# Kernel tuning notes

Measured on AMD Instinct MI355X. Metric: run time of the kernel, lower is better.

Reference implementation:

```python
import jax, jax.numpy as jnp
import numpy as np

B, T, C, H, W = 1, 8, 64, 96, 96
DG = 16  # deform groups
MAX_RES = 5.0  # max_residue_magnitude


def lrelu(x):
    return jnp.where(x >= 0, x, 0.1 * x)


def conv(x, w, b):
    y = jax.lax.conv_general_dilated(x, w, (1, 1), 'SAME',
                                     dimension_numbers=('NCHW', 'OIHW', 'NCHW'))
    return y + b[None, :, None, None]


def mod_deform_conv2d(x, offset, mask, weight, bias, dg):
    # Modulated deformable conv v2: 3x3 kernel, stride 1, pad 1, dil 1.
    Bs, Cin, Hs, Ws = x.shape
    K = 9
    cpg = Cin // dg
    Cout = weight.shape[0]
    off = offset.reshape(Bs, dg, K, 2, Hs, Ws)  # (y, x) per tap
    m = mask.reshape(Bs, dg, K, Hs, Ws)
    ky = jnp.repeat(jnp.arange(3), 3).astype(x.dtype)
    kx = jnp.tile(jnp.arange(3), 3).astype(x.dtype)
    # base sampling positions: out_pos - pad + tap*dil
    py = (jnp.arange(Hs, dtype=x.dtype) - 1.0)[None, :, None] + ky[:, None, None]  # (K,H,1)
    px = (jnp.arange(Ws, dtype=x.dtype) - 1.0)[None, None, :] + kx[:, None, None]  # (K,1,W)
    sy = off[:, :, :, 0] + py  # (B,dg,K,H,W)
    sx = off[:, :, :, 1] + px
    y0 = jnp.floor(sy)
    x0 = jnp.floor(sx)
    fy = sy - y0
    fx = sx - x0
    y0i = y0.astype(jnp.int32)
    x0i = x0.astype(jnp.int32)
    xf = x.reshape(Bs, dg, cpg, Hs * Ws)

    def gather(yi, xi, wgt):
        valid = (yi >= 0) & (yi < Hs) & (xi >= 0) & (xi < Ws)
        idx = (jnp.clip(yi, 0, Hs - 1) * Ws + jnp.clip(xi, 0, Ws - 1))
        idx = idx.reshape(Bs, dg, 1, K * Hs * Ws)
        v = jnp.take_along_axis(xf, idx, axis=3).reshape(Bs, dg, cpg, K, Hs, Ws)
        return v * (wgt * valid)[:, :, None]

    val = (gather(y0i, x0i, (1 - fy) * (1 - fx))
           + gather(y0i, x0i + 1, (1 - fy) * fx)
           + gather(y0i + 1, x0i, fy * (1 - fx))
           + gather(y0i + 1, x0i + 1, fy * fx))
    cols = val * m[:, :, None]  # (B,dg,cpg,K,H,W)
    wr = weight.reshape(Cout, dg, cpg, K)
    out = jnp.einsum('ogck,bgckhw->bohw', wr, cols)
    return out + bias[None, :, None, None]


def deform_align(xin, cond, p):
    h = lrelu(conv(cond, p['ow1'], p['ob1']))
    h = lrelu(conv(h, p['ow2'], p['ob2']))
    h = lrelu(conv(h, p['ow3'], p['ob3']))
    out = conv(h, p['ow4'], p['ob4'])
    offset = MAX_RES * jnp.tanh(out[:, :18 * DG])
    mask = jax.nn.sigmoid(out[:, 18 * DG:])
    return mod_deform_conv2d(xin, offset, mask, p['dw'], p['db'], DG)


def bidir_prop(x, params):
    t = x.shape[1]
    spatial = [x[:, i] for i in range(t)]
    feats = {}
    for name, rev in (('backward_', True), ('forward_', False)):
        p = params[name]
        order = list(range(t))[::-1] if rev else list(range(t))
        out_list = []
        prop = jnp.zeros_like(spatial[0])
        for i, idx in enumerate(order):
            cur = spatial[idx]
            if i > 0:
                feat_n2 = out_list[-2] if i > 1 else jnp.zeros_like(prop)
                cond = jnp.concatenate([prop, cur, feat_n2], axis=1)
                prop = deform_align(jnp.concatenate([prop, feat_n2], axis=1), cond, p)
            if name == 'forward_':
                feat = jnp.concatenate([cur, feats['backward_'][idx], prop], axis=1)
            else:
                feat = jnp.concatenate([cur, prop], axis=1)
            prop = prop + conv(lrelu(conv(feat, p['bw1'], p['bb1'])), p['bw2'], p['bb2'])
            out_list.append(prop)
        feats[name] = out_list[::-1] if rev else out_list
    fw, fb = params['fusion']
    outs = [conv(jnp.concatenate([feats['backward_'][i], feats['forward_'][i]], axis=1), fw, fb)
            for i in range(t)]
    return jnp.stack(outs, axis=1) + x


def setup_inputs() -> dict:
    key = jax.random.key(0)
    ks = iter(jax.random.split(key, 64))

    def w(*shape):
        return jax.random.normal(next(ks), shape, jnp.float32) * 0.03

    def b(n):
        return jnp.zeros((n,), jnp.float32)

    d = {'x': jax.random.normal(next(ks), (B, T, C, H, W), jnp.float32)}
    for pre, bb1_in in (('b', 2 * C), ('f', 3 * C)):
        d[pre + '_dw'] = w(C, 2 * C, 3, 3); d[pre + '_db'] = b(C)
        d[pre + '_ow1'] = w(C, 3 * C, 3, 3); d[pre + '_ob1'] = b(C)
        d[pre + '_ow2'] = w(C, C, 3, 3); d[pre + '_ob2'] = b(C)
        d[pre + '_ow3'] = w(C, C, 3, 3); d[pre + '_ob3'] = b(C)
        d[pre + '_ow4'] = w(27 * DG, C, 3, 3); d[pre + '_ob4'] = b(27 * DG)
        d[pre + '_bw1'] = w(C, bb1_in, 3, 3); d[pre + '_bb1'] = b(C)
        d[pre + '_bw2'] = w(C, C, 3, 3); d[pre + '_bb2'] = b(C)
    d['fus_w'] = w(C, 2 * C, 1, 1)
    d['fus_b'] = b(C)
    return d


def _assemble(b_dw, b_db, b_ow1, b_ob1, b_ow2, b_ob2, b_ow3, b_ob3, b_ow4, b_ob4,
              b_bw1, b_bb1, b_bw2, b_bb2,
              f_dw, f_db, f_ow1, f_ob1, f_ow2, f_ob2, f_ow3, f_ob3, f_ow4, f_ob4,
              f_bw1, f_bb1, f_bw2, f_bb2, fus_w, fus_b):
    return {
        'backward_': dict(dw=b_dw, db=b_db, ow1=b_ow1, ob1=b_ob1, ow2=b_ow2, ob2=b_ob2,
                          ow3=b_ow3, ob3=b_ob3, ow4=b_ow4, ob4=b_ob4,
                          bw1=b_bw1, bb1=b_bb1, bw2=b_bw2, bb2=b_bb2),
        'forward_': dict(dw=f_dw, db=f_db, ow1=f_ow1, ob1=f_ob1, ow2=f_ow2, ob2=f_ob2,
                         ow3=f_ow3, ob3=f_ob3, ow4=f_ow4, ob4=f_ob4,
                         bw1=f_bw1, bb1=f_bb1, bw2=f_bw2, bb2=f_bb2),
        'fusion': (fus_w, fus_b),
    }


def reference(x, b_dw, b_db, b_ow1, b_ob1, b_ow2, b_ob2, b_ow3, b_ob3, b_ow4, b_ob4,
              b_bw1, b_bb1, b_bw2, b_bb2,
              f_dw, f_db, f_ow1, f_ob1, f_ow2, f_ob2, f_ow3, f_ob3, f_ow4, f_ob4,
              f_bw1, f_bb1, f_bw2, f_bb2, fus_w, fus_b):
    params = _assemble(b_dw, b_db, b_ow1, b_ob1, b_ow2, b_ob2, b_ow3, b_ob3, b_ow4, b_ob4,
                       b_bw1, b_bb1, b_bw2, b_bb2,
                       f_dw, f_db, f_ow1, f_ob1, f_ow2, f_ob2, f_ow3, f_ob3, f_ow4, f_ob4,
                       f_bw1, f_bb1, f_bw2, f_bb2, fus_w, fus_b)
    return bidir_prop(x, params)
```

## Files before the change

kernel.cpp:

```cpp
#include <hip/hip_runtime.h>
#include <cstddef>
#include <cstdint>

#define HW96 9216
#define FRAME (64 * 9216)

typedef unsigned short ushort_t;
typedef __attribute__((ext_vector_type(8))) short bf16x8;
typedef __attribute__((ext_vector_type(4))) float f32x4;
typedef __attribute__((ext_vector_type(4))) unsigned u32x4;
typedef __attribute__((ext_vector_type(8))) ushort_t u16x8;
typedef __attribute__((ext_vector_type(4))) ushort_t u16x4;

__device__ __forceinline__ void split16(float v, ushort_t& h, ushort_t& l) {
    unsigned u = __float_as_uint(v);
    h = (ushort_t)(u >> 16);
    float rem = v - __uint_as_float(u & 0xFFFF0000u);
    unsigned r = __float_as_uint(rem);
    l = (ushort_t)((r + 0x7FFFu + ((r >> 16) & 1u)) >> 16);
}
__device__ __forceinline__ ushort_t bf16rnd(float v) {
    unsigned u = __float_as_uint(v);
    return (ushort_t)((u + 0x7FFFu + ((u >> 16) & 1u)) >> 16);
}
__device__ __forceinline__ float bfh(ushort_t h) {
    return __uint_as_float(((unsigned)h) << 16);
}

struct FragJob { const float* src; ushort_t* dst; int O, I, OT, KC, mode; };
struct FragJobs { FragJob j[15]; };

__global__ __launch_bounds__(256) void frag_all_k(FragJobs jobs) {
    const FragJob& J = jobs.j[blockIdx.y];
    int idx = blockIdx.x * 256 + threadIdx.x;
    int total = ((J.mode == 0) ? 9 : 1) * J.KC * J.OT * 512;
    if (idx >= total) return;
    int jj = idx & 7;
    int lane = (idx >> 3) & 63;
    int rem = idx >> 9;
    int ot = rem % J.OT;
    rem /= J.OT;
    int cc = rem % J.KC;
    int t = rem / J.KC;
    int o = ot * 16 + (lane & 15);
    float wv = 0.f;
    if (J.mode == 0) {
        int ci = cc * 32 + (lane >> 4) * 8 + jj;
        if (o < J.O && ci < J.I) wv = J.src[(o * J.I + ci) * 9 + t];
    } else if (J.mode == 1) {
        int K = cc * 32 + (lane >> 4) * 8 + jj;
        int g = K / 72, r2 = K % 72;
        int tap = r2 >> 3, c = r2 & 7;
        int ci = g * 8 + c;
        if (o < J.O && ci < J.I) wv = J.src[(o * J.I + ci) * 9 + tap];
    } else {
        int ci = cc * 32 + (lane >> 4) * 8 + jj;
        if (o < J.O && ci < J.I) wv = J.src[o * J.I + ci];
    }
    ushort_t h, l;
    split16(wv, h, l);
    J.dst[idx] = h;
    J.dst[total + idx] = l;
}

__global__ __launch_bounds__(256) void pack_tr_k(const float* __restrict__ src,
                                                 ushort_t* __restrict__ dsth) {
    const int t = blockIdx.y;
    const int px0 = blockIdx.x * 64;
    __shared__ ushort_t tile[64 * 65];
    const float* s = src + (size_t)t * FRAME;
    ushort_t* dh = dsth + (size_t)t * FRAME;
#pragma unroll
    for (int it = 0; it < 16; ++it) {
        int e = it * 256 + threadIdx.x;
        int p = e & 63, ch = e >> 6;
        tile[ch * 65 + p] = bf16rnd(s[(size_t)ch * HW96 + px0 + p]);
    }
    __syncthreads();
#pragma unroll
    for (int it = 0; it < 16; ++it) {
        int e = it * 256 + threadIdx.x;
        int ch = e & 63, p = e >> 6;
        dh[(size_t)(px0 + p) * 64 + ch] = tile[ch * 65 + p];
    }
}

__global__ __launch_bounds__(128, 3) void convh_k(
    const ushort_t* __restrict__ s0, const ushort_t* __restrict__ s1,
    const ushort_t* __restrict__ s2, int b0, int b1, int b2, int nsrc,
    const ushort_t* __restrict__ wfrag, int KCfull,
    const float* __restrict__ bias, ushort_t* __restrict__ outhi, int act) {
    const int tid = threadIdx.x;
    const int lane = tid & 63;
    const int w = tid >> 6;
    const int h = blockIdx.x & 1;
    const int bseg = blockIdx.x >> 1;
    const int ot = h * 2 + w;
    const int xb = (bseg % 6) * 16;
    const int y = bseg / 6;
    const int n = lane & 15;
    const int quad = lane >> 4;

    __shared__ __align__(16) ushort_t ldsH[3 * 18 * 72];

    int jst[4], jok[4], joff[4], jbase[4];
#pragma unroll
    for (int i = 0; i < 4; ++i) {
        int e = tid + i * 128;
        int rc = e >> 3, cg = e & 7;
        int r = rc / 18, col = rc - r * 18;
        int gy = y - 1 + r, gx = xb - 1 + col;
        jst[i] = (e < 432);
        jok[i] = jst[i] && ((unsigned)gy < 96u) && ((unsigned)gx < 96u);
        joff[i] = (gy * 96 + gx) * 64 + cg * 8;
        jbase[i] = rc * 72 + cg * 8;
    }

    f32x4 acc0, acc1;
#pragma unroll
    for (int r = 0; r < 4; ++r) { acc0[r] = 0.f; acc1[r] = 0.f; }

    for (int j = 0; j < nsrc; ++j) {
        const ushort_t* sv = (j == 0) ? s0 : (j == 1 ? s1 : s2);
        const int base = (j == 0) ? b0 : (j == 1 ? b1 : b2);
        __syncthreads();
#pragma unroll
        for (int i = 0; i < 4; ++i) {
            if (jst[i]) {
                u16x8 a;
                if (jok[i]) {
                    a = *(const u16x8*)(sv + joff[i]);
                } else {
#pragma unroll
                    for (int q = 0; q < 8; ++q) a[q] = 0;
                }
                *(u16x8*)(ldsH + jbase[i]) = a;
            }
        }
        __syncthreads();
        bf16x8 pAh[5], pBh[5];
#pragma unroll
        for (int s = 0; s < 23; ++s) {
            if (s >= 5) {
                const int u = s - 5;
                const bf16x8 Ah = pAh[u % 5];
                const bf16x8 Bh = pBh[u % 5];
                if (u & 1)
                    acc1 = __builtin_amdgcn_mfma_f32_16x16x32_bf16(Ah, Bh, acc1, 0, 0, 0);
                else
                    acc0 = __builtin_amdgcn_mfma_f32_16x16x32_bf16(Ah, Bh, acc0, 0, 0, 0);
            }
            if (s < 18) {
                const int t = s >> 1, cc2 = s & 1;
                const int ky = t / 3, kx = t % 3;
                const int ccor = base + cc2;
                const ushort_t* ab =
                    wfrag + (((size_t)(t * KCfull + ccor) * 4 + ot) * 64 + lane) * 8;
                pAh[s % 5] = *(const bf16x8*)ab;
                const int lb = (ky * 18 + n + kx) * 72 + cc2 * 32 + quad * 8;
                pBh[s % 5] = *(const bf16x8*)(ldsH + lb);
            }
        }
    }

    const int px = y * 96 + xb + n;
    u16x4 hi4;
#pragma unroll
    for (int r = 0; r < 4; ++r) {
        int cout = ot * 16 + quad * 4 + r;
        float v = acc0[r] + acc1[r] + bias[cout];
        if (act) v = (v >= 0.f) ? v : 0.1f * v;
        hi4[r] = bf16rnd(v);
    }
    *(u16x4*)(outhi + (size_t)px * 64 + ot * 16 + quad * 4) = hi4;
}

__global__ __launch_bounds__(128, 3) void convb_k(
    const ushort_t* __restrict__ s0, const ushort_t* __restrict__ s1,
    int nsrc, int dslot, const float* __restrict__ dpacc,
    const float* __restrict__ ddbias, const ushort_t* __restrict__ wfrag,
    int KCfull, const float* __restrict__ bias,
    const float* __restrict__ addsrc, const float* __restrict__ addsrc2,
    const float* __restrict__ abias, ushort_t* __restrict__ outhi, int act) {
    const int tid = threadIdx.x;
    const int lane = tid & 63;
    const int w = tid >> 6;
    const int h = blockIdx.x & 1;
    const int bseg = blockIdx.x >> 1;
    const int ot = h * 2 + w;
    const int xb = (bseg % 6) * 16;
    const int y = bseg / 6;
    const int n = lane & 15;
    const int quad = lane >> 4;

    __shared__ __align__(16) ushort_t ldsH[3 * 18 * 72];

    int jst[4], jok[4], joff[4], jbase[4];
#pragma unroll
    for (int i = 0; i < 4; ++i) {
        int e = tid + i * 128;
        int rc = e >> 3, cg = e & 7;
        int r = rc / 18, col = rc - r * 18;
        int gy = y - 1 + r, gx = xb - 1 + col;
        jst[i] = (e < 432);
        jok[i] = jst[i] && ((unsigned)gy < 96u) && ((unsigned)gx < 96u);
        joff[i] = (gy * 96 + gx) * 64 + cg * 8;
        jbase[i] = rc * 72 + cg * 8;
    }

    f32x4 acc0, acc1;
#pragma unroll
    for (int r = 0; r < 4; ++r) { acc0[r] = 0.f; acc1[r] = 0.f; }

    for (int j = 0; j < nsrc; ++j) {
        const int base = j * 2;
        __syncthreads();
        if (j == dslot) {
#pragma unroll
            for (int i = 0; i < 4; ++i) {
                if (jst[i]) {
                    u16x8 a;
                    if (jok[i]) {
                        const int cg8 = ((tid + i * 128) & 7) << 3;
                        f32x4 a0 = *(const f32x4*)(dpacc + joff[i]);
                        f32x4 a1 = *(const f32x4*)(dpacc + joff[i] + 4);
                        f32x4 b0 = *(const f32x4*)(dpacc + FRAME + joff[i]);
                        f32x4 b1 = *(const f32x4*)(dpacc + FRAME + joff[i] + 4);
                        f32x4 d0 = *(const f32x4*)(ddbias + cg8);
                        f32x4 d1 = *(const f32x4*)(ddbias + cg8 + 4);
#pragma unroll
                        for (int q = 0; q < 4; ++q) {
                            a[q] = bf16rnd(a0[q] + b0[q] + d0[q]);
                            a[4 + q] = bf16rnd(a1[q] + b1[q] + d1[q]);
                        }
                    } else {
#pragma unroll
                        for (int q = 0; q < 8; ++q) a[q] = 0;
                    }
                    *(u16x8*)(ldsH + jbase[i]) = a;
                }
            }
        } else {
            const ushort_t* sv = (j == 0) ? s0 : s1;
#pragma unroll
            for (int i = 0; i < 4; ++i) {
                if (jst[i]) {
                    u16x8 a;
                    if (jok[i]) {
                        a = *(const u16x8*)(sv + joff[i]);
                    } else {
#pragma unroll
                        for (int q = 0; q < 8; ++q) a[q] = 0;
                    }
                    *(u16x8*)(ldsH + jbase[i]) = a;
                }
            }
        }
        __syncthreads();
        bf16x8 pAh[5], pBh[5];
#pragma unroll
        for (int s = 0; s < 23; ++s) {
            if (s >= 5) {
                const int u = s - 5;
                const bf16x8 Ah = pAh[u % 5];
                const bf16x8 Bh = pBh[u % 5];
                if (u & 1)
                    acc1 = __builtin_amdgcn_mfma_f32_16x16x32_bf16(Ah, Bh, acc1, 0, 0, 0);
                else
                    acc0 = __builtin_amdgcn_mfma_f32_16x16x32_bf16(Ah, Bh, acc0, 0, 0, 0);
            }
            if (s < 18) {
                const int t = s >> 1, cc2 = s & 1;
                const int ky = t / 3, kx = t % 3;
                const int ccor = j * 2 + cc2;
                (void)ccor;
                const int cco = base + cc2;
                const ushort_t* ab =
                    wfrag + (((size_t)(t * KCfull + cco) * 4 + ot) * 64 + lane) * 8;
                pAh[s % 5] = *(const bf16x8*)ab;
                const int lb = (ky * 18 + n + kx) * 72 + cc2 * 32 + quad * 8;
                pBh[s % 5] = *(const bf16x8*)(ldsH + lb);
            }
        }
    }

    const int px = y * 96 + xb + n;
    f32x4 pa, pb;
#pragma unroll
    for (int r = 0; r < 4; ++r) { pa[r] = 0.f; pb[r] = 0.f; }
    if (addsrc) {
        pa = *(const f32x4*)(addsrc + (size_t)px * 64 + ot * 16 + quad * 4);
        pb = *(const f32x4*)(addsrc2 + (size_t)px * 64 + ot * 16 + quad * 4);
    }
    u16x4 hi4;
#pragma unroll
    for (int r = 0; r < 4; ++r) {
        int cout = ot * 16 + quad * 4 + r;
        float v = acc0[r] + acc1[r] + bias[cout];
        if (act) v = (v >= 0.f) ? v : 0.1f * v;
        if (addsrc) v += pa[r] + pb[r] + abias[cout];
        hi4[r] = bf16rnd(v);
    }
    *(u16x4*)(outhi + (size_t)px * 64 + ot * 16 + quad * 4) = hi4;
}

__global__ __launch_bounds__(256) void dconv_fused_k(
    const ushort_t* __restrict__ sAh, const ushort_t* __restrict__ sBh,
    const ushort_t* __restrict__ hAh, const ushort_t* __restrict__ w4,
    const float* __restrict__ ob4, const ushort_t* __restrict__ dwf,
    int ngr4, float* __restrict__ pacc) {
    const int tid = threadIdx.x;
    const int lane = tid & 63;
    const int w = tid >> 6;
    const int h = blockIdx.x & 1;
    const int seg = blockIdx.x >> 1;
    const int xb = (seg % 6) * 16;
    const int y = seg / 6;
    const int n = lane & 15;
    const int quad = lane >> 4;

    __shared__ __align__(16) char smem[15232 + 9472];
    float* rawS = (float*)smem;
    ushort_t* ldsAH = (ushort_t*)(smem + 15232);
    ushort_t* colsH = (ushort_t*)(smem + 15232);

    const int nrounds = ngr4 >> 1;
    const int ng = nrounds * 4;
    const int g0 = h * ng;
    const int otO_s = (g0 * 18) >> 4;
    const int otO_e = (g0 * 18 + ng * 18 - 1) >> 4;
    const int nO = otO_e - otO_s + 1;
    const int otM_s = (288 + g0 * 9) >> 4;
    const int otM_e = (288 + g0 * 9 + ng * 9 - 1) >> 4;
    const int nM = otM_e - otM_s + 1;
    const int nt = nO + nM;
    const int rowOffO = otO_s * 16;
    const int rowOffM = otM_s * 16 - nO * 16;

#pragma unroll
    for (int i = 0; i < 2; ++i) {
        int e = tid + i * 256;
        if (e < 432) {
            int rc = e >> 3, cg = e & 7;
            int r = rc / 18, col = rc - r * 18;
            int gy = y - 1 + r, gx = xb - 1 + col;
            bool ok = ((unsigned)gy < 96u) && ((unsigned)gx < 96u);
            u16x8 a;
            if (ok) {
                a = *(const u16x8*)(hAh + (gy * 96 + gx) * 64 + cg * 8);
            } else {
#pragma unroll
                for (int q = 0; q < 8; ++q) a[q] = 0;
            }
            *(u16x8*)(ldsAH + rc * 72 + cg * 8) = a;
        }
    }
    __syncthreads();

#pragma unroll 1
    for (int j = 0; j < 4; ++j) {
        const int idx = j * 4 + w;
        if (idx >= nt) break;
        const int ot = (idx < nO) ? (otO_s + idx) : (otM_s + (idx - nO));
        f32x4 a0, a1;
#pragma unroll
        for (int r = 0; r < 4; ++r) { a0[r] = 0.f; a1[r] = 0.f; }
        bf16x8 pAh[5], pBh[5];
#pragma unroll
        for (int s = 0; s < 23; ++s) {
            if (s >= 5) {
                const int u = s - 5;
                const bf16x8 Ah = pAh[u % 5];
                const bf16x8 Bh = pBh[u % 5];
                if (u & 1)
                    a1 = __builtin_amdgcn_mfma_f32_16x16x32_bf16(Ah, Bh, a1, 0, 0, 0);
                else
                    a0 = __builtin_amdgcn_mfma_f32_16x16x32_bf16(Ah, Bh, a0, 0, 0, 0);
            }
            if (s < 18) {
                const int t = s >> 1, cc2 = s & 1;
                const int ky = t / 3, kx = t % 3;
                const ushort_t* ab =
                    w4 + (((size_t)s * 28 + ot) * 64 + lane) * 8;
                pAh[s % 5] = *(const bf16x8*)ab;
                const int lb = (ky * 18 + n + kx) * 72 + cc2 * 32 + quad * 8;
                pBh[s % 5] = *(const bf16x8*)(ldsAH + lb);
            }
        }
#pragma unroll
        for (int r = 0; r < 4; ++r) {
            int cout = ot * 16 + quad * 4 + r;
            float v = a0[r] + a1[r] + (cout < 432 ? ob4[cout] : 0.f);
            rawS[(idx * 16 + quad * 4 + r) * 17 + n] = v;
        }
    }

    f32x4 acc0, acc1;
#pragma unroll
    for (int r = 0; r < 4; ++r) { acc0[r] = 0.f; acc1[r] = 0.f; }

    for (int gci = 0; gci < nrounds; ++gci) {
        const int gc = h * nrounds + gci;
        __syncthreads();
#pragma unroll
        for (int i = 0; i < 3; ++i) {
            int e = tid + i * 256;
            if (e < 576) {
                int p = e & 15;
                int r = e >> 4;
                int gl = r / 9, k = r - gl * 9;
                int g = gc * 4 + gl;
                float ry = rawS[(g * 18 + k * 2 + 0 - rowOffO) * 17 + p];
                float rx = rawS[(g * 18 + k * 2 + 1 - rowOffO) * 17 + p];
                float rm = rawS[(288 + g * 9 + k - rowOffM) * 17 + p];
                float oy = 5.f * (1.f - 2.f / (1.f + __expf(2.f * ry)));
                float ox = 5.f * (1.f - 2.f / (1.f + __expf(2.f * rx)));
                float m = 1.f / (1.f + __expf(-rm));
                float sy = oy + (float)(y - 1 + k / 3);
                float sx = ox + (float)(xb + p - 1 + k % 3);
                float fy0 = floorf(sy), fx0 = floorf(sx);
                float fy = sy - fy0, fx = sx - fx0;
                int y0 = (int)fy0, x0 = (int)fx0;
                int y1 = y0 + 1, x1 = x0 + 1;
                bool vy0 = (unsigned)y0 < 96u, vy1 = (unsigned)y1 < 96u;
                bool vx0 = (unsigned)x0 < 96u, vx1 = (unsigned)x1 < 96u;
                int cy0 = min(max(y0, 0), 95), cy1 = min(max(y1, 0), 95);
                int cx0 = min(max(x0, 0), 95), cx1 = min(max(x1, 0), 95);
                float w00 = (1.f - fy) * (1.f - fx) * ((vy0 && vx0) ? 1.f : 0.f);
                float w01 = (1.f - fy) * fx * ((vy0 && vx1) ? 1.f : 0.f);
                float w10 = fy * (1.f - fx) * ((vy1 && vx0) ? 1.f : 0.f);
                float w11 = fy * fx * ((vy1 && vx1) ? 1.f : 0.f);
                const ushort_t* src = (g < 8) ? sAh : sBh;
                int cb = (g & 7) * 8;
                int kbase = p * 296 + gl * 72 + k * 8;
                ushort_t hh[8];
                if (src) {
                    u16x8 c00 = *(const u16x8*)(src + (cy0 * 96 + cx0) * 64 + cb);
                    u16x8 c01 = *(const u16x8*)(src + (cy0 * 96 + cx1) * 64 + cb);
                    u16x8 c10 = *(const u16x8*)(src + (cy1 * 96 + cx0) * 64 + cb);
                    u16x8 c11 = *(const u16x8*)(src + (cy1 * 96 + cx1) * 64 + cb);
#pragma unroll
                    for (int c = 0; c < 8; ++c) {
                        float v = w00 * bfh(c00[c]) + w01 * bfh(c01[c]) +
                                  w10 * bfh(c10[c]) + w11 * bfh(c11[c]);
                        hh[c] = bf16rnd(v * m);
                    }
                } else {
#pragma unroll
                    for (int c = 0; c < 8; ++c) hh[c] = 0;
                }
                u32x4 H;
#pragma unroll
                for (int q = 0; q < 4; ++q)
                    H[q] = (unsigned)hh[2 * q] | ((unsigned)hh[2 * q + 1] << 16);
                *(u32x4*)(colsH + kbase) = H;
            }
        }
        __syncthreads();
        bf16x8 qAh[4], qBh[4];
#pragma unroll
        for (int s = 0; s < 13; ++s) {
            if (s >= 4) {
                const int u = s - 4;
                const bf16x8 Ah = qAh[u % 4];
                const bf16x8 Bh = qBh[u % 4];
                if (u & 1)
                    acc1 = __builtin_amdgcn_mfma_f32_16x16x32_bf16(Ah, Bh, acc1, 0, 0, 0);
                else
                    acc0 = __builtin_amdgcn_mfma_f32_16x16x32_bf16(Ah, Bh, acc0, 0, 0, 0);
            }
            if (s < 9) {
                const int cc = gc * 9 + s;
                const ushort_t* ab = dwf + (((size_t)cc * 4 + w) * 64 + lane) * 8;
                qAh[s % 4] = *(const bf16x8*)ab;
                const int lb = n * 296 + s * 32 + quad * 8;
                qBh[s % 4] = *(const bf16x8*)(colsH + lb);
            }
        }
    }

    const int pidx = y * 96 + xb + n;
    f32x4 sv;
#pragma unroll
    for (int r = 0; r < 4; ++r) sv[r] = acc0[r] + acc1[r];
    *(f32x4*)(pacc + (size_t)h * FRAME + (size_t)pidx * 64 + w * 16 +
              quad * 4) = sv;
}

__global__ __launch_bounds__(128) void fusem_k(
    const ushort_t* __restrict__ featBh, const ushort_t* __restrict__ featFh,
    const float* __restrict__ x, const ushort_t* __restrict__ wfrag,
    const float* __restrict__ bias, float* __restrict__ out) {
    const int tid = threadIdx.x;
    const int lane = tid & 63;
    const int w = tid >> 6;
    const int h = blockIdx.x & 1;
    const int bseg = blockIdx.x >> 1;
    const int t = blockIdx.y;
    const int ot = h * 2 + w;
    const int xb = (bseg % 6) * 16;
    const int y = bseg / 6;
    const int n = lane & 15;
    const int quad = lane >> 4;

    __shared__ __align__(16) ushort_t ldsH[16 * 144];

    const int p = tid >> 3, cg = tid & 7;
    const int off = ((y * 96 + xb + p) * 64 + cg * 8);
#pragma unroll
    for (int i = 0; i < 2; ++i) {
        const ushort_t* sv =
            (i == 0 ? featBh : featFh) + (size_t)t * FRAME;
        u16x8 a = *(const u16x8*)(sv + off);
        *(u16x8*)(ldsH + p * 144 + i * 64 + cg * 8) = a;
    }
    __syncthreads();

    f32x4 acc0, acc1;
#pragma unroll
    for (int r = 0; r < 4; ++r) { acc0[r] = 0.f; acc1[r] = 0.f; }
    const size_t hlOff = (size_t)4 * 4 * 512;
#pragma unroll
    for (int cc = 0; cc < 4; ++cc) {
        const ushort_t* ab = wfrag + (((size_t)cc * 4 + ot) * 64 + lane) * 8;
        bf16x8 Ah = *(const bf16x8*)ab;
        bf16x8 Al = *(const bf16x8*)(ab + hlOff);
        int lb = n * 144 + cc * 32 + quad * 8;
        bf16x8 Bh = *(const bf16x8*)(ldsH + lb);
        if (cc & 1) {
            acc1 = __builtin_amdgcn_mfma_f32_16x16x32_bf16(Ah, Bh, acc1, 0, 0, 0);
            acc1 = __builtin_amdgcn_mfma_f32_16x16x32_bf16(Al, Bh, acc1, 0, 0, 0);
        } else {
            acc0 = __builtin_amdgcn_mfma_f32_16x16x32_bf16(Ah, Bh, acc0, 0, 0, 0);
            acc0 = __builtin_amdgcn_mfma_f32_16x16x32_bf16(Al, Bh, acc0, 0, 0, 0);
        }
    }

    const int pidx = y * 96 + xb + n;
    const float* xt = x + (size_t)t * FRAME;
    float* od = out + (size_t)t * FRAME;
#pragma unroll
    for (int r = 0; r < 4; ++r) {
        int cout = ot * 16 + quad * 4 + r;
        size_t o2 = (size_t)cout * HW96 + pidx;
        od[o2] = acc0[r] + acc1[r] + bias[cout] + xt[o2];
    }
}

extern "C" void kernel_launch(void* const* d_in, const int* in_sizes, int n_in,
                              void* d_out, int out_size, void* d_ws,
                              size_t ws_size, hipStream_t stream) {
    const float* x = (const float*)d_in[0];
    auto gp = [&](int i) { return (const float*)d_in[i]; };

    struct DirP {
        const float *dw, *db, *ow1, *ob1, *ow2, *ob2, *ow3, *ob3, *ow4, *ob4,
            *bw1, *bb1, *bw2, *bb2;
    };
    DirP Pb{gp(1), gp(2), gp(3), gp(4), gp(5), gp(6), gp(7),
            gp(8), gp(9), gp(10), gp(11), gp(12), gp(13), gp(14)};
    DirP Pf{gp(15), gp(16), gp(17), gp(18), gp(19), gp(20), gp(21),
            gp(22), gp(23), gp(24), gp(25), gp(26), gp(27), gp(28)};
    const float* fus_w = gp(29);
    const float* fus_b = gp(30);

    ushort_t* xh = (ushort_t*)d_ws;
    ushort_t* featBh = xh + (size_t)8 * FRAME;
    ushort_t* featFh = featBh + (size_t)8 * FRAME;
    ushort_t* hAh = featFh + (size_t)8 * FRAME;
    ushort_t* hBh = hAh + FRAME;
    float* pacc = (float*)((((uintptr_t)(hBh + FRAME)) + 15) & ~(uintptr_t)15);
    ushort_t* fragp = (ushort_t*)(pacc + (size_t)2 * FRAME);

    auto falloc = [&](size_t nelem) {
        ushort_t* p = fragp;
        fragp += nelem;
        return p;
    };

    struct DirW { ushort_t *ow1, *ow2, *ow3, *ow4, *bw1, *bw2, *dw; int bw1KC; };
    FragJobs fj;
    int nf = 0;
    auto fjob = [&](const float* src, int O, int I, int OT, int KC) {
        ushort_t* dst = falloc((size_t)2 * 9 * KC * OT * 512);
        fj.j[nf++] = FragJob{src, dst, O, I, OT, KC, 0};
        return dst;
    };
    auto fjobd = [&](const float* src) {
        ushort_t* dst = falloc((size_t)2 * 36 * 4 * 512);
        fj.j[nf++] = FragJob{src, dst, 64, 128, 4, 36, 1};
        return dst;
    };
    DirW Wb, Wf;
    Wb.ow1 = fjob(Pb.ow1, 64, 192, 4, 6);
    Wb.ow2 = fjob(Pb.ow2, 64, 64, 4, 2);
    Wb.ow3 = fjob(Pb.ow3, 64, 64, 4, 2);
    Wb.ow4 = fjob(Pb.ow4, 432, 64, 28, 2);
    Wb.bw1 = fjob(Pb.bw1, 64, 128, 4, 4);
    Wb.bw1KC = 4;
    Wb.bw2 = fjob(Pb.bw2, 64, 64, 4, 2);
    Wb.dw = fjobd(Pb.dw);
    Wf.ow1 = fjob(Pf.ow1, 64, 192, 4, 6);
    Wf.ow2 = fjob(Pf.ow2, 64, 64, 4, 2);
    Wf.ow3 = fjob(Pf.ow3, 64, 64, 4, 2);
    Wf.ow4 = fjob(Pf.ow4, 432, 64, 28, 2);
    Wf.bw1 = fjob(Pf.bw1, 64, 192, 4, 6);
    Wf.bw1KC = 6;
    Wf.bw2 = fjob(Pf.bw2, 64, 64, 4, 2);
    Wf.dw = fjobd(Pf.dw);
    ushort_t* Wfus = falloc((size_t)2 * 4 * 4 * 512);
    fj.j[nf++] = FragJob{fus_w, Wfus, 64, 128, 4, 4, 2};
    frag_all_k<<<dim3(1008, 15), 256, 0, stream>>>(fj);

    pack_tr_k<<<dim3(144, 8), 256, 0, stream>>>(x, xh);

    auto convh = [&](const ushort_t* a, const ushort_t* b, const ushort_t* c2,
                     const ushort_t* frag, int KCfull, const float* bias,
                     ushort_t* out, int act) {
        const ushort_t* srcs[3] = {a, b, c2};
        const ushort_t* S[3] = {nullptr, nullptr, nullptr};
        int B[3] = {0, 0, 0};
        int ns = 0;
        for (int j = 0; j < 3; ++j)
            if (srcs[j]) {
                S[ns] = srcs[j];
                B[ns] = j * 2;
                ++ns;
            }
        convh_k<<<1152, 128, 0, stream>>>(S[0], S[1], S[2], B[0], B[1], B[2],
                                          ns, frag, KCfull, bias, out, act);
    };

    auto convb = [&](const ushort_t* a, const ushort_t* b, int withD,
                     const float* ddbias, const ushort_t* frag, int KCfull,
                     const float* bias, const float* add, const float* add2,
                     const float* abias, ushort_t* out, int act) {
        const ushort_t* S[2] = {nullptr, nullptr};
        int ns = 0;
        if (a) S[ns++] = a;
        if (b) S[ns++] = b;
        int dslot = -1;
        if (withD) { dslot = ns; ++ns; }
        convb_k<<<1152, 128, 0, stream>>>(S[0], S[1], ns, dslot, pacc, ddbias,
                                          frag, KCfull, bias, add, add2,
                                          abias, out, act);
    };

    for (int dir = 0; dir < 2; ++dir) {
        const DirP& P = dir ? Pf : Pb;
        const DirW& W = dir ? Wf : Wb;
        ushort_t* feath = dir ? featFh : featBh;
        const ushort_t* prev1h = nullptr;
        const ushort_t* prev2h = nullptr;
        for (int i = 0; i < 8; ++i) {
            int idx = dir ? i : 7 - i;
            const ushort_t* curh = xh + (size_t)idx * FRAME;
            bool hasD = false;
            if (i > 0) {
                convh(prev1h, curh, prev2h, W.ow1, 6, P.ob1, hAh, 1);
                convh(hAh, nullptr, nullptr, W.ow2, 2, P.ob2, hBh, 1);
                convh(hBh, nullptr, nullptr, W.ow3, 2, P.ob3, hAh, 1);
                int ngr4 = (prev2h != nullptr) ? 4 : 2;
                dconv_fused_k<<<1152, 256, 0, stream>>>(
                    prev1h, prev2h, hAh, W.ow4, P.ob4, W.dw, ngr4, pacc);
                hasD = true;
            }
            ushort_t* dsth = feath + (size_t)idx * FRAME;
            if (dir == 0) {
                convb(curh, nullptr, hasD ? 1 : 0, P.db, W.bw1, W.bw1KC,
                      P.bb1, nullptr, nullptr, nullptr, hBh, 1);
            } else {
                convb(curh, featBh + (size_t)idx * FRAME, hasD ? 1 : 0, P.db,
                      W.bw1, W.bw1KC, P.bb1, nullptr, nullptr, nullptr, hBh,
                      1);
            }
            convb(hBh, nullptr, 0, nullptr, W.bw2, 2, P.bb2,
                  hasD ? pacc : nullptr, pacc + FRAME, P.db, dsth, 0);
            prev2h = prev1h;
            prev1h = dsth;
        }
    }

    fusem_k<<<dim3(1152, 8), 128, 0, stream>>>(featBh, featFh, x, Wfus,
                                               fus_b, (float*)d_out);
}
```

Baseline: 1.063 ms.

## Split deform conv across one block per group-chunk with per-chunk partial buffers

The fused deformable conv kernel now launches one block per 4-group chunk (576*ngr4 blocks) instead of two blocks that each loop over several chunks. Each block computes only the offset/mask tiles it needs and writes its own partial sum buffer. The downstream conv kernels then sum a variable number of partials, and the pacc buffer grows to four frames. This adds parallelism and cuts LDS per block, at the cost of redundant loading and offset-conv work per block and more partial reads downstream.

```diff
diff --git a/kernel.cpp b/kernel.cpp
--- a/kernel.cpp
+++ b/kernel.cpp
@@ -177,10 +177,9 @@
 
 __global__ __launch_bounds__(128, 3) void convb_k(
     const ushort_t* __restrict__ s0, const ushort_t* __restrict__ s1,
-    int nsrc, int dslot, const float* __restrict__ dpacc,
+    int nsrc, int dslot, const float* __restrict__ dpacc, int npacc,
     const float* __restrict__ ddbias, const ushort_t* __restrict__ wfrag,
-    int KCfull, const float* __restrict__ bias,
-    const float* __restrict__ addsrc, const float* __restrict__ addsrc2,
+    int KCfull, const float* __restrict__ bias, int addn,
     const float* __restrict__ abias, ushort_t* __restrict__ outhi, int act) {
     const int tid = threadIdx.x;
     const int lane = tid & 63;
@@ -222,16 +221,17 @@
                     u16x8 a;
                     if (jok[i]) {
                         const int cg8 = ((tid + i * 128) & 7) << 3;
-                        f32x4 a0 = *(const f32x4*)(dpacc + joff[i]);
-                        f32x4 a1 = *(const f32x4*)(dpacc + joff[i] + 4);
-                        f32x4 b0 = *(const f32x4*)(dpacc + FRAME + joff[i]);
-                        f32x4 b1 = *(const f32x4*)(dpacc + FRAME + joff[i] + 4);
-                        f32x4 d0 = *(const f32x4*)(ddbias + cg8);
-                        f32x4 d1 = *(const f32x4*)(ddbias + cg8 + 4);
+                        f32x4 v0 = *(const f32x4*)(ddbias + cg8);
+                        f32x4 v1 = *(const f32x4*)(ddbias + cg8 + 4);
+                        for (int q2 = 0; q2 < npacc; ++q2) {
+                            const float* pq = dpacc + (size_t)q2 * FRAME;
+                            v0 += *(const f32x4*)(pq + joff[i]);
+                            v1 += *(const f32x4*)(pq + joff[i] + 4);
+                        }
 #pragma unroll
                         for (int q = 0; q < 4; ++q) {
-                            a[q] = bf16rnd(a0[q] + b0[q] + d0[q]);
-                            a[4 + q] = bf16rnd(a1[q] + b1[q] + d1[q]);
+                            a[q] = bf16rnd(v0[q]);
+                            a[4 + q] = bf16rnd(v1[q]);
                         }
                     } else {
 #pragma unroll
@@ -272,8 +272,6 @@
             if (s < 18) {
                 const int t = s >> 1, cc2 = s & 1;
                 const int ky = t / 3, kx = t % 3;
-                const int ccor = j * 2 + cc2;
-                (void)ccor;
                 const int cco = base + cc2;
                 const ushort_t* ab =
                     wfrag + (((size_t)(t * KCfull + cco) * 4 + ot) * 64 + lane) * 8;
@@ -285,12 +283,13 @@
     }
 
     const int px = y * 96 + xb + n;
-    f32x4 pa, pb;
-#pragma unroll
-    for (int r = 0; r < 4; ++r) { pa[r] = 0.f; pb[r] = 0.f; }
-    if (addsrc) {
-        pa = *(const f32x4*)(addsrc + (size_t)px * 64 + ot * 16 + quad * 4);
-        pb = *(const f32x4*)(addsrc2 + (size_t)px * 64 + ot * 16 + quad * 4);
+    f32x4 pa;
+#pragma unroll
+    for (int r = 0; r < 4; ++r) pa[r] = 0.f;
+    if (addn) {
+        const size_t eo = (size_t)px * 64 + ot * 16 + quad * 4;
+        for (int q2 = 0; q2 < addn; ++q2)
+            pa += *(const f32x4*)(dpacc + (size_t)q2 * FRAME + eo);
     }
     u16x4 hi4;
 #pragma unroll
@@ -298,7 +297,7 @@
         int cout = ot * 16 + quad * 4 + r;
         float v = acc0[r] + acc1[r] + bias[cout];
         if (act) v = (v >= 0.f) ? v : 0.1f * v;
-        if (addsrc) v += pa[r] + pb[r] + abias[cout];
+        if (addn) v += pa[r] + abias[cout];
         hi4[r] = bf16rnd(v);
     }
     *(u16x4*)(outhi + (size_t)px * 64 + ot * 16 + quad * 4) = hi4;
@@ -312,26 +311,24 @@
     const int tid = threadIdx.x;
     const int lane = tid & 63;
     const int w = tid >> 6;
-    const int h = blockIdx.x & 1;
-    const int seg = blockIdx.x >> 1;
+    const int gc = blockIdx.x % ngr4;
+    const int seg = blockIdx.x / ngr4;
     const int xb = (seg % 6) * 16;
     const int y = seg / 6;
     const int n = lane & 15;
     const int quad = lane >> 4;
 
-    __shared__ __align__(16) char smem[15232 + 9472];
+    __shared__ __align__(16) char smem[8704 + 9472];
     float* rawS = (float*)smem;
-    ushort_t* ldsAH = (ushort_t*)(smem + 15232);
-    ushort_t* colsH = (ushort_t*)(smem + 15232);
-
-    const int nrounds = ngr4 >> 1;
-    const int ng = nrounds * 4;
-    const int g0 = h * ng;
+    ushort_t* ldsAH = (ushort_t*)(smem + 8704);
+    ushort_t* colsH = (ushort_t*)(smem + 8704);
+
+    const int g0 = gc * 4;
     const int otO_s = (g0 * 18) >> 4;
-    const int otO_e = (g0 * 18 + ng * 18 - 1) >> 4;
+    const int otO_e = (g0 * 18 + 71) >> 4;
     const int nO = otO_e - otO_s + 1;
     const int otM_s = (288 + g0 * 9) >> 4;
-    const int otM_e = (288 + g0 * 9 + ng * 9 - 1) >> 4;
+    const int otM_e = (288 + g0 * 9 + 35) >> 4;
     const int nM = otM_e - otM_s + 1;
     const int nt = nO + nM;
     const int rowOffO = otO_s * 16;
@@ -358,7 +355,7 @@
     __syncthreads();
 
 #pragma unroll 1
-    for (int j = 0; j < 4; ++j) {
+    for (int j = 0; j < 2; ++j) {
         const int idx = j * 4 + w;
         if (idx >= nt) break;
         const int ot = (idx < nO) ? (otO_s + idx) : (otM_s + (idx - nO));
@@ -399,83 +396,80 @@
 #pragma unroll
     for (int r = 0; r < 4; ++r) { acc0[r] = 0.f; acc1[r] = 0.f; }
 
-    for (int gci = 0; gci < nrounds; ++gci) {
-        const int gc = h * nrounds + gci;
-        __syncthreads();
-#pragma unroll
-        for (int i = 0; i < 3; ++i) {
-            int e = tid + i * 256;
-            if (e < 576) {
-                int p = e & 15;
-                int r = e >> 4;
-                int gl = r / 9, k = r - gl * 9;
-                int g = gc * 4 + gl;
-                float ry = rawS[(g * 18 + k * 2 + 0 - rowOffO) * 17 + p];
-                float rx = rawS[(g * 18 + k * 2 + 1 - rowOffO) * 17 + p];
-                float rm = rawS[(288 + g * 9 + k - rowOffM) * 17 + p];
-                float oy = 5.f * (1.f - 2.f / (1.f + __expf(2.f * ry)));
-                float ox = 5.f * (1.f - 2.f / (1.f + __expf(2.f * rx)));
-                float m = 1.f / (1.f + __expf(-rm));
-                float sy = oy + (float)(y - 1 + k / 3);
-                float sx = ox + (float)(xb + p - 1 + k % 3);
-                float fy0 = floorf(sy), fx0 = floorf(sx);
-                float fy = sy - fy0, fx = sx - fx0;
-                int y0 = (int)fy0, x0 = (int)fx0;
-                int y1 = y0 + 1, x1 = x0 + 1;
-                bool vy0 = (unsigned)y0 < 96u, vy1 = (unsigned)y1 < 96u;
-                bool vx0 = (unsigned)x0 < 96u, vx1 = (unsigned)x1 < 96u;
-                int cy0 = min(max(y0, 0), 95), cy1 = min(max(y1, 0), 95);
-                int cx0 = min(max(x0, 0), 95), cx1 = min(max(x1, 0), 95);
-                float w00 = (1.f - fy) * (1.f - fx) * ((vy0 && vx0) ? 1.f : 0.f);
-                float w01 = (1.f - fy) * fx * ((vy0 && vx1) ? 1.f : 0.f);
-                float w10 = fy * (1.f - fx) * ((vy1 && vx0) ? 1.f : 0.f);
-                float w11 = fy * fx * ((vy1 && vx1) ? 1.f : 0.f);
-                const ushort_t* src = (g < 8) ? sAh : sBh;
-                int cb = (g & 7) * 8;
-                int kbase = p * 296 + gl * 72 + k * 8;
-                ushort_t hh[8];
-                if (src) {
-                    u16x8 c00 = *(const u16x8*)(src + (cy0 * 96 + cx0) * 64 + cb);
-                    u16x8 c01 = *(const u16x8*)(src + (cy0 * 96 + cx1) * 64 + cb);
-                    u16x8 c10 = *(const u16x8*)(src + (cy1 * 96 + cx0) * 64 + cb);
-                    u16x8 c11 = *(const u16x8*)(src + (cy1 * 96 + cx1) * 64 + cb);
-#pragma unroll
-                    for (int c = 0; c < 8; ++c) {
-                        float v = w00 * bfh(c00[c]) + w01 * bfh(c01[c]) +
-                                  w10 * bfh(c10[c]) + w11 * bfh(c11[c]);
-                        hh[c] = bf16rnd(v * m);
-                    }
-                } else {
-#pragma unroll
-                    for (int c = 0; c < 8; ++c) hh[c] = 0;
+    __syncthreads();
+#pragma unroll
+    for (int i = 0; i < 3; ++i) {
+        int e = tid + i * 256;
+        if (e < 576) {
+            int p = e & 15;
+            int r = e >> 4;
+            int gl = r / 9, k = r - gl * 9;
+            int g = gc * 4 + gl;
+            float ry = rawS[(g * 18 + k * 2 + 0 - rowOffO) * 17 + p];
+            float rx = rawS[(g * 18 + k * 2 + 1 - rowOffO) * 17 + p];
+            float rm = rawS[(288 + g * 9 + k - rowOffM) * 17 + p];
+            float oy = 5.f * (1.f - 2.f / (1.f + __expf(2.f * ry)));
+            float ox = 5.f * (1.f - 2.f / (1.f + __expf(2.f * rx)));
+            float m = 1.f / (1.f + __expf(-rm));
+            float sy = oy + (float)(y - 1 + k / 3);
+            float sx = ox + (float)(xb + p - 1 + k % 3);
+            float fy0 = floorf(sy), fx0 = floorf(sx);
+            float fy = sy - fy0, fx = sx - fx0;
+            int y0 = (int)fy0, x0 = (int)fx0;
+            int y1 = y0 + 1, x1 = x0 + 1;
+            bool vy0 = (unsigned)y0 < 96u, vy1 = (unsigned)y1 < 96u;
+            bool vx0 = (unsigned)x0 < 96u, vx1 = (unsigned)x1 < 96u;
+            int cy0 = min(max(y0, 0), 95), cy1 = min(max(y1, 0), 95);
+            int cx0 = min(max(x0, 0), 95), cx1 = min(max(x1, 0), 95);
+            float w00 = (1.f - fy) * (1.f - fx) * ((vy0 && vx0) ? 1.f : 0.f);
+            float w01 = (1.f - fy) * fx * ((vy0 && vx1) ? 1.f : 0.f);
+            float w10 = fy * (1.f - fx) * ((vy1 && vx0) ? 1.f : 0.f);
+            float w11 = fy * fx * ((vy1 && vx1) ? 1.f : 0.f);
+            const ushort_t* src = (g < 8) ? sAh : sBh;
+            int cb = (g & 7) * 8;
+            int kbase = p * 296 + gl * 72 + k * 8;
+            ushort_t hh[8];
+            if (src) {
+                u16x8 c00 = *(const u16x8*)(src + (cy0 * 96 + cx0) * 64 + cb);
+                u16x8 c01 = *(const u16x8*)(src + (cy0 * 96 + cx1) * 64 + cb);
+                u16x8 c10 = *(const u16x8*)(src + (cy1 * 96 + cx0) * 64 + cb);
+                u16x8 c11 = *(const u16x8*)(src + (cy1 * 96 + cx1) * 64 + cb);
+#pragma unroll
+                for (int c = 0; c < 8; ++c) {
+                    float v = w00 * bfh(c00[c]) + w01 * bfh(c01[c]) +
+                              w10 * bfh(c10[c]) + w11 * bfh(c11[c]);
+                    hh[c] = bf16rnd(v * m);
                 }
-                u32x4 H;
-#pragma unroll
-                for (int q = 0; q < 4; ++q)
-                    H[q] = (unsigned)hh[2 * q] | ((unsigned)hh[2 * q + 1] << 16);
-                *(u32x4*)(colsH + kbase) = H;
-            }
-        }
-        __syncthreads();
-        bf16x8 qAh[4], qBh[4];
-#pragma unroll
-        for (int s = 0; s < 13; ++s) {
-            if (s >= 4) {
-                const int u = s - 4;
-                const bf16x8 Ah = qAh[u % 4];
-                const bf16x8 Bh = qBh[u % 4];
-                if (u & 1)
-                    acc1 = __builtin_amdgcn_mfma_f32_16x16x32_bf16(Ah, Bh, acc1, 0, 0, 0);
-                else
-                    acc0 = __builtin_amdgcn_mfma_f32_16x16x32_bf16(Ah, Bh, acc0, 0, 0, 0);
-            }
-            if (s < 9) {
-                const int cc = gc * 9 + s;
-                const ushort_t* ab = dwf + (((size_t)cc * 4 + w) * 64 + lane) * 8;
-                qAh[s % 4] = *(const bf16x8*)ab;
-                const int lb = n * 296 + s * 32 + quad * 8;
-                qBh[s % 4] = *(const bf16x8*)(colsH + lb);
-            }
+            } else {
+#pragma unroll
+                for (int c = 0; c < 8; ++c) hh[c] = 0;
+            }
+            u32x4 H;
+#pragma unroll
+            for (int q = 0; q < 4; ++q)
+                H[q] = (unsigned)hh[2 * q] | ((unsigned)hh[2 * q + 1] << 16);
+            *(u32x4*)(colsH + kbase) = H;
+        }
+    }
+    __syncthreads();
+    bf16x8 qAh[4], qBh[4];
+#pragma unroll
+    for (int s = 0; s < 13; ++s) {
+        if (s >= 4) {
+            const int u = s - 4;
+            const bf16x8 Ah = qAh[u % 4];
+            const bf16x8 Bh = qBh[u % 4];
+            if (u & 1)
+                acc1 = __builtin_amdgcn_mfma_f32_16x16x32_bf16(Ah, Bh, acc1, 0, 0, 0);
+            else
+                acc0 = __builtin_amdgcn_mfma_f32_16x16x32_bf16(Ah, Bh, acc0, 0, 0, 0);
+        }
+        if (s < 9) {
+            const int cc = gc * 9 + s;
+            const ushort_t* ab = dwf + (((size_t)cc * 4 + w) * 64 + lane) * 8;
+            qAh[s % 4] = *(const bf16x8*)ab;
+            const int lb = n * 296 + s * 32 + quad * 8;
+            qBh[s % 4] = *(const bf16x8*)(colsH + lb);
         }
     }
 
@@ -483,7 +477,7 @@
     f32x4 sv;
 #pragma unroll
     for (int r = 0; r < 4; ++r) sv[r] = acc0[r] + acc1[r];
-    *(f32x4*)(pacc + (size_t)h * FRAME + (size_t)pidx * 64 + w * 16 +
+    *(f32x4*)(pacc + (size_t)gc * FRAME + (size_t)pidx * 64 + w * 16 +
               quad * 4) = sv;
 }
 
@@ -570,7 +564,7 @@
     ushort_t* hAh = featFh + (size_t)8 * FRAME;
     ushort_t* hBh = hAh + FRAME;
     float* pacc = (float*)((((uintptr_t)(hBh + FRAME)) + 15) & ~(uintptr_t)15);
-    ushort_t* fragp = (ushort_t*)(pacc + (size_t)2 * FRAME);
+    ushort_t* fragp = (ushort_t*)(pacc + (size_t)4 * FRAME);
 
     auto falloc = [&](size_t nelem) {
         ushort_t* p = fragp;
@@ -632,8 +626,8 @@
     };
 
     auto convb = [&](const ushort_t* a, const ushort_t* b, int withD,
-                     const float* ddbias, const ushort_t* frag, int KCfull,
-                     const float* bias, const float* add, const float* add2,
+                     int npacc, const float* ddbias, const ushort_t* frag,
+                     int KCfull, const float* bias, int addn,
                      const float* abias, ushort_t* out, int act) {
         const ushort_t* S[2] = {nullptr, nullptr};
         int ns = 0;
@@ -641,8 +635,8 @@
         if (b) S[ns++] = b;
         int dslot = -1;
         if (withD) { dslot = ns; ++ns; }
-        convb_k<<<1152, 128, 0, stream>>>(S[0], S[1], ns, dslot, pacc, ddbias,
-                                          frag, KCfull, bias, add, add2,
+        convb_k<<<1152, 128, 0, stream>>>(S[0], S[1], ns, dslot, pacc, npacc,
+                                          ddbias, frag, KCfull, bias, addn,
                                           abias, out, act);
     };
 
@@ -655,27 +649,25 @@
         for (int i = 0; i < 8; ++i) {
             int idx = dir ? i : 7 - i;
             const ushort_t* curh = xh + (size_t)idx * FRAME;
-            bool hasD = false;
+            int ngr4 = 0;
             if (i > 0) {
                 convh(prev1h, curh, prev2h, W.ow1, 6, P.ob1, hAh, 1);
                 convh(hAh, nullptr, nullptr, W.ow2, 2, P.ob2, hBh, 1);
                 convh(hBh, nullptr, nullptr, W.ow3, 2, P.ob3, hAh, 1);
-                int ngr4 = (prev2h != nullptr) ? 4 : 2;
-                dconv_fused_k<<<1152, 256, 0, stream>>>(
+                ngr4 = (prev2h != nullptr) ? 4 : 2;
+                dconv_fused_k<<<576 * ngr4, 256, 0, stream>>>(
                     prev1h, prev2h, hAh, W.ow4, P.ob4, W.dw, ngr4, pacc);
-                hasD = true;
             }
             ushort_t* dsth = feath + (size_t)idx * FRAME;
             if (dir == 0) {
-                convb(curh, nullptr, hasD ? 1 : 0, P.db, W.bw1, W.bw1KC,
-                      P.bb1, nullptr, nullptr, nullptr, hBh, 1);
+                convb(curh, nullptr, ngr4 ? 1 : 0, ngr4, P.db, W.bw1,
+                      W.bw1KC, P.bb1, 0, nullptr, hBh, 1);
             } else {
-                convb(curh, featBh + (size_t)idx * FRAME, hasD ? 1 : 0, P.db,
-                      W.bw1, W.bw1KC, P.bb1, nullptr, nullptr, nullptr, hBh,
-                      1);
-            }
-            convb(hBh, nullptr, 0, nullptr, W.bw2, 2, P.bb2,
-                  hasD ? pacc : nullptr, pacc + FRAME, P.db, dsth, 0);
+                convb(curh, featBh + (size_t)idx * FRAME, ngr4 ? 1 : 0, ngr4,
+                      P.db, W.bw1, W.bw1KC, P.bb1, 0, nullptr, hBh, 1);
+            }
+            convb(hBh, nullptr, 0, 0, nullptr, W.bw2, 2, P.bb2, ngr4, P.db,
+                  dsth, 0);
             prev2h = prev1h;
             prev1h = dsth;
         }
```

New measurement: 1.155 ms. 1.09x slower.
